# Optimization experiments

Measured on AMD Instinct MI355X. Metric: run time of the kernel, lower is better.

## Reference

```python
import jax, jax.numpy as jnp
import numpy as np

IN_C, OUT_C, K = 256, 256, 3

def setup_inputs() -> dict:
    key = jax.random.key(0)
    kx, kw, kb = jax.random.split(key, 3)
    x = jax.random.normal(kx, (32, IN_C, 56, 56), dtype=jnp.float32)
    # kaiming-like scale for conv weight
    fan_in = IN_C * K * K
    weight = jax.random.normal(kw, (OUT_C, IN_C, K, K), dtype=jnp.float32) / np.sqrt(fan_in)
    bias = jax.random.normal(kb, (OUT_C,), dtype=jnp.float32) * 0.01
    return {"x": x, "weight": weight, "bias": bias}

def reference(x, weight, bias):
    # SparseConv2d computes an (approximately lossless, threshold=1e-6)
    # block-sparse conv2d; exact math == dense conv2d, stride 1, pad 1.
    y = jax.lax.conv_general_dilated(
        x, weight,
        window_strides=(1, 1),
        padding=((1, 1), (1, 1)),
        dimension_numbers=("NCHW", "OIHW", "NCHW"),
    )
    return y + bias[None, :, None, None]
```

## Files before the change

### kernel.cpp

```cpp
#include <hip/hip_runtime.h>
#include <hip/hip_bf16.h>

#define IN_C  256
#define OUT_C 256
#define HH 56
#define WW 56
#define NN 32
#define XT_H 58
#define XT_W 64
#define WT_BYTES (8*9*256*32*2)

#define XS_BYTES 24576
#define LDS_TOTAL (2*XS_BYTES)

using short8 = __attribute__((ext_vector_type(8))) short;
using f32x4  = __attribute__((ext_vector_type(4))) float;

__device__ __forceinline__ void gload_lds16(const void* g, void* l) {
  __builtin_amdgcn_global_load_lds((const __attribute__((address_space(1))) void*)g,
                                   (__attribute__((address_space(3))) void*)l,
                                   16, 0, 0);
}

#define VMWAIT(N) asm volatile("s_waitcnt vmcnt(" #N ")" ::: "memory")

__global__ void k_prep(const float* __restrict__ x, const float* __restrict__ w,
                       __hip_bfloat16* __restrict__ wt, __hip_bfloat16* __restrict__ xt) {
  const int b = blockIdx.x, tid = threadIdx.x;

  if (b >= NN * XT_H) {
    const int base = (b - NN * XT_H) * 1024;
#pragma unroll
    for (int k = 0; k < 4; ++k) {
      int idx = base + k * 256 + tid;
      int kw = idx % 3; int t1 = idx / 3;
      int kh = t1 % 3;  int t2 = t1 / 3;
      int ic = t2 % IN_C; int oc = t2 / IN_C;
      int tap = kh * 3 + kw;
      wt[((((ic >> 5) * 9 + tap) * 256 + oc) * 32) + (ic & 31)] = __float2bfloat16(w[idx]);
    }
    return;
  }

  const int n = b / XT_H, hp = b % XT_H;
  __hip_bfloat16* row = xt + (size_t)(n * XT_H + hp) * XT_W * 256;

  if (hp == 0 || hp == XT_H - 1) {
    int4 z; z.x = z.y = z.z = z.w = 0;
#pragma unroll
    for (int k = 0; k < 8; ++k) ((int4*)row)[k * 256 + tid] = z;
    return;
  }

  const int h = hp - 1;
  __shared__ __hip_bfloat16 tile[56][264];

  {
    const int ic = tid;
    const float* src = x + (((size_t)n * IN_C + ic) * HH + h) * WW;
#pragma unroll
    for (int j = 0; j < 14; ++j) {
      float4 v = ((const float4*)src)[j];
      tile[4 * j + 0][ic] = __float2bfloat16(v.x);
      tile[4 * j + 1][ic] = __float2bfloat16(v.y);
      tile[4 * j + 2][ic] = __float2bfloat16(v.z);
      tile[4 * j + 3][ic] = __float2bfloat16(v.w);
    }
  }
  {
    int4 z; z.x = z.y = z.z = z.w = 0;
    int cell = tid >> 5, s = tid & 31;
    int wp = (cell == 0) ? 0 : (56 + cell);
    ((int4*)(row + (size_t)wp * 256))[s] = z;
  }
  __syncthreads();
#pragma unroll
  for (int k = 0; k < 7; ++k) {
    int e = k * 256 + tid;
    int wq = e >> 5, seg = e & 31;
    short8 v = *(const short8*)&tile[wq][seg * 8];
    *(short8*)(row + (size_t)(wq + 1) * 256 + seg * 8) = v;
  }
}

__global__ __launch_bounds__(256, 2) void k_conv(
    const __hip_bfloat16* __restrict__ wt, const __hip_bfloat16* __restrict__ xt,
    const float* __restrict__ bias, float* __restrict__ out) {
  extern __shared__ __align__(16) char lds[];
  char* xs_c = lds;

  const int tid  = threadIdx.x;
  const int wid  = tid >> 6, lane = tid & 63;
  const int cc   = lane & 15, g = lane >> 4;
  const int wn   = wid & 1,  wm = wid >> 1;

  const int work = (blockIdx.x & 7) * 112 + (blockIdx.x >> 3);
  const int n  = work / 28;
  const int rem = work - n * 28;
  const int q  = rem >> 1, oh = rem & 1;
  const int h0 = q * 4;

  int xoff[7];
#pragma unroll
  for (int pt = 0; pt < 7; ++pt) {
    int p = wm * 112 + pt * 16 + cc;
    int rp = p / 56, wp = p - rp * 56;
    xoff[pt] = rp * 4096 + wp * 64 + g * 16;
  }
  const int ocb = oh * 128 + wn * 64;
  const __hip_bfloat16* wlane = wt + (size_t)(ocb + cc) * 32 + g * 8;

  f32x4 acc[4][7];
#pragma unroll
  for (int a = 0; a < 4; ++a)
#pragma unroll
    for (int bb = 0; bb < 7; ++bb) acc[a][bb] = (f32x4){0.f, 0.f, 0.f, 0.f};

  const __hip_bfloat16* xtn = xt + (size_t)(n * XT_H + h0) * XT_W * 256;

  auto stage_x = [&](int buf, int ch) {
#pragma unroll
    for (int i = 0; i < 6; ++i) {
      int s = wid * 6 + i;
      int rowc = s >> 2, colq = s & 3;
      const __hip_bfloat16* src = xtn + (size_t)(rowc * 64 + colq * 16 + (lane >> 2)) * 256
                                      + ch * 32 + (lane & 3) * 8;
      gload_lds16(src, xs_c + buf * XS_BYTES + rowc * 4096 + colq * 1024);
    }
  };
  auto loadw1 = [&](int ph, int oct) -> short8 {
    return *(const short8*)(wlane + (size_t)ph * 8192 + oct * 512);
  };

  short8 wA, wB, wC;

  stage_x(0, 0);
  __builtin_amdgcn_sched_barrier(0);
  wA = loadw1(0, 0);
  wB = loadw1(0, 1);

#define MFMA7(W_, oct_) do {                                                          \
    __builtin_amdgcn_s_setprio(1);                                                    \
    _Pragma("unroll")                                                                 \
    for (int pt = 0; pt < 7; ++pt)                                                    \
      acc[oct_][pt] = __builtin_amdgcn_mfma_f32_16x16x32_bf16(W_, xf[pt], acc[oct_][pt], 0, 0, 0); \
    __builtin_amdgcn_s_setprio(0);                                                    \
  } while (0)

#define PHASE(ph_, kh_, kw_, T0_, T1_, T2_) do {                                      \
    short8 xf[7];                                                                     \
    _Pragma("unroll")                                                                 \
    for (int pt = 0; pt < 7; ++pt)                                                    \
      xf[pt] = *(const short8*)(xb + xoff[pt] + (kh_) * 4096 + (kw_) * 64);           \
    T2_ = loadw1(ph_, 2);                                                             \
    MFMA7(T0_, 0);                                                                    \
    T0_ = loadw1(ph_, 3);                                                             \
    MFMA7(T1_, 1);                                                                    \
    T1_ = loadw1((ph_) + 1, 0);                                                       \
    MFMA7(T2_, 2);                                                                    \
    T2_ = loadw1((ph_) + 1, 1);                                                       \
    MFMA7(T0_, 3);                                                                    \
  } while (0)

  for (int ch = 0; ch < 8; ++ch) {
    if (ch == 0) { VMWAIT(2); } else { VMWAIT(8); }
    __builtin_amdgcn_s_barrier();
    if (ch < 7) {
      stage_x((ch + 1) & 1, ch + 1);
      __builtin_amdgcn_sched_barrier(0);
    }
    const char* xb = xs_c + ((ch & 1) ? XS_BYTES : 0);
    const int ph0 = ch * 9;
    PHASE(ph0 + 0, 0, 0, wA, wB, wC);
    PHASE(ph0 + 1, 0, 1, wB, wC, wA);
    PHASE(ph0 + 2, 0, 2, wC, wA, wB);
    PHASE(ph0 + 3, 1, 0, wA, wB, wC);
    PHASE(ph0 + 4, 1, 1, wB, wC, wA);
    PHASE(ph0 + 5, 1, 2, wC, wA, wB);
    PHASE(ph0 + 6, 2, 0, wA, wB, wC);
    PHASE(ph0 + 7, 2, 1, wB, wC, wA);
    PHASE(ph0 + 8, 2, 2, wC, wA, wB);
  }
#undef PHASE
#undef MFMA7

  int rp_[7], wp_[7];
#pragma unroll
  for (int pt = 0; pt < 7; ++pt) {
    int p = wm * 112 + pt * 16 + cc;
    rp_[pt] = p / 56; wp_[pt] = p - rp_[pt] * 56;
  }
#pragma unroll
  for (int oct = 0; oct < 4; ++oct) {
    const int oc0 = ocb + oct * 16 + 4 * g;
#pragma unroll
    for (int r = 0; r < 4; ++r) {
      const float bv = bias[oc0 + r];
      const size_t obase = ((size_t)n * OUT_C + (oc0 + r)) * (HH * WW);
#pragma unroll
      for (int pt = 0; pt < 7; ++pt)
        out[obase + (size_t)(h0 + rp_[pt]) * 56 + wp_[pt]] = acc[oct][pt][r] + bv;
    }
  }
}

extern "C" void kernel_launch(void* const* d_in, const int* in_sizes, int n_in,
                              void* d_out, int out_size, void* d_ws, size_t ws_size,
                              hipStream_t stream) {
  const float* x    = (const float*)d_in[0];
  const float* w    = (const float*)d_in[1];
  const float* bias = (const float*)d_in[2];
  float* out        = (float*)d_out;

  __hip_bfloat16* wt = (__hip_bfloat16*)d_ws;
  __hip_bfloat16* xt = (__hip_bfloat16*)((char*)d_ws + WT_BYTES);

  hipFuncSetAttribute((const void*)k_conv,
                      hipFuncAttributeMaxDynamicSharedMemorySize, LDS_TOTAL);

  k_prep<<<NN * XT_H + 576, 256, 0, stream>>>(x, w, wt, xt);
  k_conv<<<NN * 14 * 2, 256, LDS_TOTAL, stream>>>(wt, xt, bias, out);
}
```

Baseline: 138.1 us.

## Swizzle LDS input tile to avoid bank conflicts and deepen weight prefetch

```diff
diff --git a/kernel.cpp b/kernel.cpp
--- a/kernel.cpp
+++ b/kernel.cpp
@@ -100,13 +100,16 @@
   const int q  = rem >> 1, oh = rem & 1;
   const int h0 = q * 4;
 
-  int xoff[7];
-#pragma unroll
-  for (int pt = 0; pt < 7; ++pt) {
-    int p = wm * 112 + pt * 16 + cc;
-    int rp = p / 56, wp = p - rp * 56;
-    xoff[pt] = rp * 4096 + wp * 64 + g * 16;
-  }
+  int xoffk[3][7];
+#pragma unroll
+  for (int kw = 0; kw < 3; ++kw)
+#pragma unroll
+    for (int pt = 0; pt < 7; ++pt) {
+      int p = wm * 112 + pt * 16 + cc;
+      int rp = p / 56, wp = p - rp * 56;
+      int col = wp + kw;
+      xoffk[kw][pt] = rp * 4096 + col * 64 + (((g + (col >> 1)) & 3) * 16);
+    }
   const int ocb = oh * 128 + wn * 64;
   const __hip_bfloat16* wlane = wt + (size_t)(ocb + cc) * 32 + g * 8;
 
@@ -118,13 +121,14 @@
 
   const __hip_bfloat16* xtn = xt + (size_t)(n * XT_H + h0) * XT_W * 256;
 
+  const int glog = ((lane & 3) - (lane >> 3)) & 3;
   auto stage_x = [&](int buf, int ch) {
 #pragma unroll
     for (int i = 0; i < 6; ++i) {
       int s = wid * 6 + i;
       int rowc = s >> 2, colq = s & 3;
       const __hip_bfloat16* src = xtn + (size_t)(rowc * 64 + colq * 16 + (lane >> 2)) * 256
-                                      + ch * 32 + (lane & 3) * 8;
+                                      + ch * 32 + glog * 8;
       gload_lds16(src, xs_c + buf * XS_BYTES + rowc * 4096 + colq * 1024);
     }
   };
@@ -132,38 +136,39 @@
     return *(const short8*)(wlane + (size_t)ph * 8192 + oct * 512);
   };
 
-  short8 wA, wB, wC;
+  short8 wA, wB, wC, wD;
 
   stage_x(0, 0);
   __builtin_amdgcn_sched_barrier(0);
   wA = loadw1(0, 0);
   wB = loadw1(0, 1);
-
-#define MFMA7(W_, oct_) do {                                                          \
+  wC = loadw1(0, 2);
+
+#define MFMA7(X_, W_, oct_) do {                                                      \
     __builtin_amdgcn_s_setprio(1);                                                    \
     _Pragma("unroll")                                                                 \
     for (int pt = 0; pt < 7; ++pt)                                                    \
-      acc[oct_][pt] = __builtin_amdgcn_mfma_f32_16x16x32_bf16(W_, xf[pt], acc[oct_][pt], 0, 0, 0); \
+      acc[oct_][pt] = __builtin_amdgcn_mfma_f32_16x16x32_bf16(W_, X_[pt], acc[oct_][pt], 0, 0, 0); \
     __builtin_amdgcn_s_setprio(0);                                                    \
   } while (0)
 
-#define PHASE(ph_, kh_, kw_, T0_, T1_, T2_) do {                                      \
+#define PHASE(ph_, kh_, kw_) do {                                                     \
     short8 xf[7];                                                                     \
     _Pragma("unroll")                                                                 \
     for (int pt = 0; pt < 7; ++pt)                                                    \
-      xf[pt] = *(const short8*)(xb + xoff[pt] + (kh_) * 4096 + (kw_) * 64);           \
-    T2_ = loadw1(ph_, 2);                                                             \
-    MFMA7(T0_, 0);                                                                    \
-    T0_ = loadw1(ph_, 3);                                                             \
-    MFMA7(T1_, 1);                                                                    \
-    T1_ = loadw1((ph_) + 1, 0);                                                       \
-    MFMA7(T2_, 2);                                                                    \
-    T2_ = loadw1((ph_) + 1, 1);                                                       \
-    MFMA7(T0_, 3);                                                                    \
+      xf[pt] = *(const short8*)(xb + xoffk[kw_][pt] + (kh_) * 4096);                  \
+    wD = loadw1(ph_, 3);                                                              \
+    MFMA7(xf, wA, 0);                                                                 \
+    wA = loadw1((ph_) + 1, 0);                                                        \
+    MFMA7(xf, wB, 1);                                                                 \
+    wB = loadw1((ph_) + 1, 1);                                                        \
+    MFMA7(xf, wC, 2);                                                                 \
+    wC = loadw1((ph_) + 1, 2);                                                        \
+    MFMA7(xf, wD, 3);                                                                 \
   } while (0)
 
   for (int ch = 0; ch < 8; ++ch) {
-    if (ch == 0) { VMWAIT(2); } else { VMWAIT(8); }
+    VMWAIT(3);
     __builtin_amdgcn_s_barrier();
     if (ch < 7) {
       stage_x((ch + 1) & 1, ch + 1);
@@ -171,15 +176,15 @@
     }
     const char* xb = xs_c + ((ch & 1) ? XS_BYTES : 0);
     const int ph0 = ch * 9;
-    PHASE(ph0 + 0, 0, 0, wA, wB, wC);
-    PHASE(ph0 + 1, 0, 1, wB, wC, wA);
-    PHASE(ph0 + 2, 0, 2, wC, wA, wB);
-    PHASE(ph0 + 3, 1, 0, wA, wB, wC);
-    PHASE(ph0 + 4, 1, 1, wB, wC, wA);
-    PHASE(ph0 + 5, 1, 2, wC, wA, wB);
-    PHASE(ph0 + 6, 2, 0, wA, wB, wC);
-    PHASE(ph0 + 7, 2, 1, wB, wC, wA);
-    PHASE(ph0 + 8, 2, 2, wC, wA, wB);
+    PHASE(ph0 + 0, 0, 0);
+    PHASE(ph0 + 1, 0, 1);
+    PHASE(ph0 + 2, 0, 2);
+    PHASE(ph0 + 3, 1, 0);
+    PHASE(ph0 + 4, 1, 1);
+    PHASE(ph0 + 5, 1, 2);
+    PHASE(ph0 + 6, 2, 0);
+    PHASE(ph0 + 7, 2, 1);
+    PHASE(ph0 + 8, 2, 2);
   }
 #undef PHASE
 #undef MFMA7
```

Result: slower. 145.0 us (+5.0%).
